# Kernel optimization log

Measured on AMD Instinct MI355X. Metric: run time of the kernel, lower is better.

## Reference

```python
import jax, jax.numpy as jnp
import numpy as np


def setup_inputs() -> dict:
    key = jax.random.key(0)
    k1, k2, k3, k4, k5 = jax.random.split(key, 5)
    B, S, H, NL = 256, 128, 768, 2
    return {
        "t_logits": jax.random.normal(k1, (B, NL), dtype=jnp.float32),
        "s_logits": jax.random.normal(k2, (B, NL), dtype=jnp.float32),
        "t_features": jax.random.normal(k3, (B, S, H), dtype=jnp.float32),
        "s_features": jax.random.normal(k4, (B, S, H), dtype=jnp.float32),
        "labels": jax.random.randint(k5, (B,), 0, NL, dtype=jnp.int64),
        "k": 5,
        "temperature": 4,
    }


def reference(t_logits, s_logits, t_features, s_features, labels, k, temperature):
    B = s_features.shape[0]
    D = s_features.shape[1] * s_features.shape[2]  # flattened feature dim S*H
    T = jnp.asarray(temperature, dtype=s_logits.dtype)

    # train_loss: standard cross-entropy computed inside the student model
    logp = jax.nn.log_softmax(s_logits, axis=-1)
    train_loss = -jnp.mean(jnp.take_along_axis(logp, labels[:, None].astype(jnp.int32), axis=1))

    # soft_loss: KL(batchmean) between temperature-softened teacher/student
    soft_targets = jax.nn.softmax(t_logits / T, axis=-1)
    log_probs = jax.nn.log_softmax(s_logits / T, axis=-1)
    soft_loss = jnp.sum(soft_targets * (jnp.log(soft_targets) - log_probs)) / B * T * T

    # distill_loss: per-sample squared distances to label-matched teacher
    # features, take k nearest (self included, dist 0), sum of per-neighbor
    # MSE = sqdist / D.
    tf = t_features.reshape(B, -1)
    sf = s_features.reshape(B, -1)
    # ||s_i - t_j||^2 via GEMM: [B, B]
    sq = (jnp.sum(sf * sf, axis=1)[:, None]
          + jnp.sum(tf * tf, axis=1)[None, :]
          - 2.0 * sf @ tf.T)
    sq = jnp.maximum(sq, 0.0)
    same = labels[:, None] == labels[None, :]
    masked = jnp.where(same, sq, jnp.inf)
    neg_top, _ = jax.lax.top_k(-masked, k)  # k smallest distances per row
    vals = -neg_top
    valid = jnp.isfinite(vals)  # handles groups smaller than k
    distill_loss = jnp.sum(jnp.where(valid, vals, 0.0)) / D

    return train_loss, soft_loss, distill_loss
```

## Files before the change

### kernel.cpp

```cpp
#include <hip/hip_runtime.h>
#include <math.h>


#define BMAC 256
#define BKF  32
#define LP   32
#define ST   (BMAC * LP)

typedef __attribute__((ext_vector_type(8))) short short8;
typedef __attribute__((ext_vector_type(4))) float f32x4;

__device__ inline unsigned pack_bf16(float a, float b) {
    unsigned ua = __float_as_uint(a), ub = __float_as_uint(b);
    ua = (ua + 0x7fffu + ((ua >> 16) & 1u)) >> 16;
    ub = (ub + 0x7fffu + ((ub >> 16) & 1u)) >> 16;
    return (ua & 0xffffu) | (ub << 16);
}

__global__ __launch_bounds__(1024) void gemm_dot_kernel(const float* __restrict__ S,
                                                        const float* __restrict__ T,
                                                        float* __restrict__ part,
                                                        float* __restrict__ spart,
                                                        float* __restrict__ tpart,
                                                        int* __restrict__ counter,
                                                        int B, int K, int KC) {
    extern __shared__ __align__(16) unsigned short smem[];

    const int tid  = threadIdx.x;
    const int bz   = blockIdx.x;
    const int kbeg = bz * KC;
    const int iters = KC / BKF;

    if (bz == 0 && tid == 0) *counter = 0;

    const int r = tid >> 2;
    const int g = tid & 3;
    int gi = r < B ? r : B - 1;
    const float* srcS = S + (size_t)gi * K + kbeg + g * 8;
    const float* srcT = T + (size_t)gi * K + kbeg + g * 8;
    const int woff = r * LP + ((g ^ (r & 3)) * 8);

    const int lane = tid & 63;
    const int wid  = tid >> 6;
    const int wm   = wid >> 2;
    const int wn   = wid & 3;
    const int l15  = lane & 15;
    const int quad = lane >> 4;
    const int xq   = (quad ^ (l15 & 3)) * 8;
    int aoff[4], boff[4];
    #pragma unroll
    for (int t = 0; t < 4; ++t) {
        aoff[t] = (wm * 64 + t * 16 + l15) * LP + xq;
        boff[t] = (wn * 64 + t * 16 + l15) * LP + xq;
    }

    f32x4 acc[4][4] = {};
    float pns = 0.f, pnt = 0.f;

    f32x4 s0 = *(const f32x4*)srcS;
    f32x4 s1 = *(const f32x4*)(srcS + 4);
    f32x4 t0 = *(const f32x4*)srcT;
    f32x4 t1 = *(const f32x4*)(srcT + 4);

    for (int it = 0; it < iters; ++it) {
        unsigned short* As = smem + (it & 1) * 2 * ST;
        unsigned short* Bs = As + ST;

        pns += s0.x*s0.x + s0.y*s0.y + s0.z*s0.z + s0.w*s0.w
             + s1.x*s1.x + s1.y*s1.y + s1.z*s1.z + s1.w*s1.w;
        pnt += t0.x*t0.x + t0.y*t0.y + t0.z*t0.z + t0.w*t0.w
             + t1.x*t1.x + t1.y*t1.y + t1.z*t1.z + t1.w*t1.w;
        uint4 pa = make_uint4(pack_bf16(s0.x, s0.y), pack_bf16(s0.z, s0.w),
                              pack_bf16(s1.x, s1.y), pack_bf16(s1.z, s1.w));
        uint4 pb = make_uint4(pack_bf16(t0.x, t0.y), pack_bf16(t0.z, t0.w),
                              pack_bf16(t1.x, t1.y), pack_bf16(t1.z, t1.w));
        *(uint4*)&As[woff] = pa;
        *(uint4*)&Bs[woff] = pb;

        if (it + 1 < iters) {
            const float* nS = srcS + (it + 1) * BKF;
            const float* nT = srcT + (it + 1) * BKF;
            s0 = *(const f32x4*)nS;
            s1 = *(const f32x4*)(nS + 4);
            t0 = *(const f32x4*)nT;
            t1 = *(const f32x4*)(nT + 4);
        }

        __syncthreads();

        short8 bfr[4];
        #pragma unroll
        for (int ni = 0; ni < 4; ++ni)
            bfr[ni] = *(const short8*)&Bs[boff[ni]];
        #pragma unroll
        for (int mi = 0; mi < 4; ++mi) {
            short8 afr = *(const short8*)&As[aoff[mi]];
            #pragma unroll
            for (int ni = 0; ni < 4; ++ni)
                acc[mi][ni] = __builtin_amdgcn_mfma_f32_16x16x32_bf16(
                    afr, bfr[ni], acc[mi][ni], 0, 0, 0);
        }
    }

    float* outp = part + (size_t)bz * B * B;
    #pragma unroll
    for (int mi = 0; mi < 4; ++mi) {
        #pragma unroll
        for (int ni = 0; ni < 4; ++ni) {
            #pragma unroll
            for (int rr = 0; rr < 4; ++rr) {
                const int ig = wm * 64 + mi * 16 + quad * 4 + rr;
                const int jg = wn * 64 + ni * 16 + l15;
                if (ig < B && jg < B)
                    outp[(size_t)ig * B + jg] = acc[mi][ni][rr];
            }
        }
    }

    {
        float v = pns;
        v += __shfl_xor(v, 1, 64);
        v += __shfl_xor(v, 2, 64);
        if ((tid & 3) == 0 && r < B) spart[(size_t)bz * B + r] = v;
        float w = pnt;
        w += __shfl_xor(w, 1, 64);
        w += __shfl_xor(w, 2, 64);
        if ((tid & 3) == 0 && r < B) tpart[(size_t)bz * B + r] = w;
    }
}

__global__ __launch_bounds__(256) void tail_kernel(const float* __restrict__ part,
                                                   const float* __restrict__ spart,
                                                   const float* __restrict__ tpart,
                                                   const float* __restrict__ t_logits,
                                                   const float* __restrict__ s_logits,
                                                   const int* __restrict__ labels,
                                                   const int* __restrict__ kp,
                                                   const int* __restrict__ tp,
                                                   float* __restrict__ rowsum,
                                                   int* __restrict__ counter,
                                                   float* __restrict__ out,
                                                   int B, int K, int NL, int gz) {
    const int i   = blockIdx.x;
    const int tid = threadIdx.x;
    const size_t BB = (size_t)B * B;

    __shared__ float svals[256];
    __shared__ float rv[256];
    __shared__ int   ri[256];
    __shared__ float red[4];
    __shared__ float snv;
    __shared__ int   lastf;

    float sp = 0.f;
    for (int z = tid; z < gz; z += 256) sp += spart[(size_t)z * B + i];
    #pragma unroll
    for (int off = 32; off > 0; off >>= 1) sp += __shfl_down(sp, off, 64);
    if ((tid & 63) == 0) red[tid >> 6] = sp;
    __syncthreads();
    if (tid == 0) snv = red[0] + red[1] + red[2] + red[3];
    __syncthreads();
    const float sn = snv;

    float v = INFINITY;
    if (tid < B) {
        const float* pp = part + (size_t)i * B + tid;
        const float* tq = tpart + tid;
        float d0=0.f,d1=0.f,d2=0.f,d3=0.f,d4=0.f,d5=0.f,d6=0.f,d7=0.f;
        float tn = 0.f;
        int z = 0;
        for (; z + 8 <= gz; z += 8) {
            d0 += pp[(size_t)(z+0) * BB];
            d1 += pp[(size_t)(z+1) * BB];
            d2 += pp[(size_t)(z+2) * BB];
            d3 += pp[(size_t)(z+3) * BB];
            d4 += pp[(size_t)(z+4) * BB];
            d5 += pp[(size_t)(z+5) * BB];
            d6 += pp[(size_t)(z+6) * BB];
            d7 += pp[(size_t)(z+7) * BB];
            tn += tq[(size_t)(z+0) * B] + tq[(size_t)(z+1) * B]
                + tq[(size_t)(z+2) * B] + tq[(size_t)(z+3) * B]
                + tq[(size_t)(z+4) * B] + tq[(size_t)(z+5) * B]
                + tq[(size_t)(z+6) * B] + tq[(size_t)(z+7) * B];
        }
        float dt = ((d0+d1)+(d2+d3)) + ((d4+d5)+(d6+d7));
        for (; z < gz; ++z) {
            dt += pp[(size_t)z * BB];
            tn += tq[(size_t)z * B];
        }
        if (labels[i] == labels[tid])
            v = fmaxf(sn + tn - 2.0f * dt, 0.0f);
    }
    svals[tid] = v;
    __syncthreads();

    const int k = kp[0];
    float sum = 0.0f;
    for (int it = 0; it < k; ++it) {
        rv[tid] = svals[tid];
        ri[tid] = tid;
        __syncthreads();
        #pragma unroll
        for (int s = 128; s > 0; s >>= 1) {
            if (tid < s) {
                if (rv[tid + s] < rv[tid]) { rv[tid] = rv[tid + s]; ri[tid] = ri[tid + s]; }
            }
            __syncthreads();
        }
        if (tid == 0) {
            if (rv[0] < 3.0e38f) sum += rv[0];
            svals[ri[0]] = INFINITY;
        }
        __syncthreads();
    }

    if (tid == 0) {
        rowsum[i] = sum;
        __threadfence();
        lastf = (atomicAdd(counter, 1) == B - 1) ? 1 : 0;
    }
    __syncthreads();
    if (!lastf) return;

    __threadfence();
    const float Tv = (float)tp[0];
    float rs = (tid < B) ? rowsum[tid] : 0.f;
    float ce = 0.0f, kl = 0.0f;
    for (int s = tid; s < B; s += 256) {
        const float* sl = s_logits + (size_t)s * NL;
        const float* tl = t_logits + (size_t)s * NL;
        float mx = -INFINITY;
        for (int c = 0; c < NL; ++c) mx = fmaxf(mx, sl[c]);
        float se = 0.0f;
        for (int c = 0; c < NL; ++c) se += expf(sl[c] - mx);
        ce += logf(se) + mx - sl[labels[s]];

        float mxs = -INFINITY, mxt = -INFINITY;
        for (int c = 0; c < NL; ++c) {
            mxs = fmaxf(mxs, sl[c] / Tv);
            mxt = fmaxf(mxt, tl[c] / Tv);
        }
        float ses = 0.0f, set = 0.0f;
        for (int c = 0; c < NL; ++c) {
            ses += expf(sl[c] / Tv - mxs);
            set += expf(tl[c] / Tv - mxt);
        }
        float lses = logf(ses) + mxs;
        float lset = logf(set) + mxt;
        for (int c = 0; c < NL; ++c) {
            float lst = tl[c] / Tv - lset;
            float ls  = sl[c] / Tv - lses;
            kl += expf(lst) * (lst - ls);
        }
    }
    #pragma unroll
    for (int off = 32; off > 0; off >>= 1) {
        ce += __shfl_down(ce, off, 64);
        kl += __shfl_down(kl, off, 64);
        rs += __shfl_down(rs, off, 64);
    }
    __shared__ float wce[4], wkl[4], wrs[4];
    if ((tid & 63) == 0) { wce[tid >> 6] = ce; wkl[tid >> 6] = kl; wrs[tid >> 6] = rs; }
    __syncthreads();
    if (tid == 0) {
        out[0] = (wce[0] + wce[1] + wce[2] + wce[3]) / (float)B;
        out[1] = (wkl[0] + wkl[1] + wkl[2] + wkl[3]) / (float)B * Tv * Tv;
        out[2] = (wrs[0] + wrs[1] + wrs[2] + wrs[3]) / (float)K;
    }
}

extern "C" void kernel_launch(void* const* d_in, const int* in_sizes, int n_in,
                              void* d_out, int out_size, void* d_ws, size_t ws_size,
                              hipStream_t stream) {
    const float* t_logits = (const float*)d_in[0];
    const float* s_logits = (const float*)d_in[1];
    const float* t_feat   = (const float*)d_in[2];
    const float* s_feat   = (const float*)d_in[3];
    const int*   labels   = (const int*)d_in[4];
    const int*   kp       = (const int*)d_in[5];
    const int*   tp       = (const int*)d_in[6];
    float* out = (float*)d_out;

    const int B  = in_sizes[4];
    const int NL = in_sizes[0] / B;
    const int K  = in_sizes[2] / B;
    const size_t BB = (size_t)B * B;

    const size_t avail = ws_size / 4;
    const int cands[] = {256, 192, 128, 96, 64, 48, 32, 24, 16, 12, 8, 6, 4};
    int gz = 4;
    for (int ci = 0; ci < 13; ++ci) {
        const int g = cands[ci];
        if (K % (g * BKF) != 0) continue;
        const size_t need = (size_t)g * BB + 2 * (size_t)g * B + B + 1;
        if (need <= avail) { gz = g; break; }
    }
    const int KC = K / gz;

    float* ws      = (float*)d_ws;
    float* part    = ws;
    float* spart   = part + (size_t)gz * BB;
    float* tpart   = spart + (size_t)gz * B;
    float* rowsum  = tpart + (size_t)gz * B;
    int*   counter = (int*)(rowsum + B);

    const size_t lds_bytes = 2 * 2 * (size_t)ST * sizeof(unsigned short);
    gemm_dot_kernel<<<gz, 1024, lds_bytes, stream>>>(s_feat, t_feat, part,
                                                     spart, tpart, counter,
                                                     B, K, KC);

    tail_kernel<<<B, 256, 0, stream>>>(part, spart, tpart, t_logits, s_logits,
                                       labels, kp, tp, rowsum, counter, out,
                                       B, K, NL, gz);
}
```

Baseline: 276.1 us.

## Tile split-K GEMM into 128x128 output blocks with XCD-aware scheduling

Replaces the one-block-per-K-slice 256x256 GEMM (1024 threads) with 128x128 output tiles handled by 256-thread blocks, so the grid becomes tiles x split-K. This raises block count and occupancy (launch bounds of 3 blocks per CU), and maps K slices to XCDs so blocks sharing inputs land on the same L2. Row norms are computed only by the tiles on the first row or column. LDS now uses padded rows (stride 40) in place of the XOR swizzle. The cost is that each input row is loaded twice across tiles, and gz drops from 256 to 192.

```diff
diff --git a/kernel.cpp b/kernel.cpp
--- a/kernel.cpp
+++ b/kernel.cpp
@@ -2,10 +2,11 @@
 #include <math.h>
 
 
-#define BMAC 256
-#define BKF  32
-#define LP   32
-#define ST   (BMAC * LP)
+#define TM 128
+#define TN 128
+#define BK 32
+#define LP 40
+#define STH (TM * LP)
 
 typedef __attribute__((ext_vector_type(8))) short short8;
 typedef __attribute__((ext_vector_type(4))) float f32x4;
@@ -17,73 +18,113 @@
     return (ua & 0xffffu) | (ub << 16);
 }
 
-__global__ __launch_bounds__(1024) void gemm_dot_kernel(const float* __restrict__ S,
-                                                        const float* __restrict__ T,
-                                                        float* __restrict__ part,
-                                                        float* __restrict__ spart,
-                                                        float* __restrict__ tpart,
-                                                        int* __restrict__ counter,
-                                                        int B, int K, int KC) {
+__global__ __launch_bounds__(256, 3) void gemm_dot_kernel(const float* __restrict__ S,
+                                                          const float* __restrict__ T,
+                                                          float* __restrict__ part,
+                                                          float* __restrict__ spart,
+                                                          float* __restrict__ tpart,
+                                                          int* __restrict__ counter,
+                                                          int B, int K, int KC,
+                                                          int mt, int nt, int gz) {
     extern __shared__ __align__(16) unsigned short smem[];
 
-    const int tid  = threadIdx.x;
-    const int bz   = blockIdx.x;
-    const int kbeg = bz * KC;
-    const int iters = KC / BKF;
-
-    if (bz == 0 && tid == 0) *counter = 0;
-
-    const int r = tid >> 2;
-    const int g = tid & 3;
-    int gi = r < B ? r : B - 1;
-    const float* srcS = S + (size_t)gi * K + kbeg + g * 8;
-    const float* srcT = T + (size_t)gi * K + kbeg + g * 8;
-    const int woff = r * LP + ((g ^ (r & 3)) * 8);
+    const int tid   = threadIdx.x;
+    const int blk   = blockIdx.x;
+    const int tiles = mt * nt;
+
+    if (blk == 0 && tid == 0) *counter = 0;
+
+    int z, mn;
+    if ((gz & 7) == 0) {
+        const int xcd  = blk & 7;
+        const int slot = blk >> 3;
+        const int zpx  = gz >> 3;
+        mn = slot % tiles;
+        z  = xcd * zpx + slot / tiles;
+    } else {
+        z  = blk / tiles;
+        mn = blk % tiles;
+    }
+    const int i0 = (mn / nt) * TM;
+    const int j0 = (mn % nt) * TN;
+    const int kbeg  = z * KC;
+    const int iters = KC / BK;
 
     const int lane = tid & 63;
     const int wid  = tid >> 6;
-    const int wm   = wid >> 2;
-    const int wn   = wid & 3;
+    const int wm   = wid >> 1;
+    const int wn   = wid & 1;
     const int l15  = lane & 15;
     const int quad = lane >> 4;
-    const int xq   = (quad ^ (l15 & 3)) * 8;
+
+    const int r = tid >> 1;
+    const int h = tid & 1;
+    int gi = i0 + r; if (gi >= B) gi = B - 1;
+    int gj = j0 + r; if (gj >= B) gj = B - 1;
+    const float* srcS = S + (size_t)gi * K + kbeg + h * 16;
+    const float* srcT = T + (size_t)gj * K + kbeg + h * 16;
+    const int woff = r * LP + h * 16;
+
     int aoff[4], boff[4];
     #pragma unroll
     for (int t = 0; t < 4; ++t) {
-        aoff[t] = (wm * 64 + t * 16 + l15) * LP + xq;
-        boff[t] = (wn * 64 + t * 16 + l15) * LP + xq;
-    }
+        aoff[t] = (wm * 64 + t * 16 + l15) * LP + quad * 8;
+        boff[t] = (wn * 64 + t * 16 + l15) * LP + quad * 8;
+    }
+
+    const bool doS = ((mn % nt) == 0);
+    const bool doT = ((mn / nt) == 0);
 
     f32x4 acc[4][4] = {};
     float pns = 0.f, pnt = 0.f;
 
-    f32x4 s0 = *(const f32x4*)srcS;
+    f32x4 s0 = *(const f32x4*)(srcS + 0);
     f32x4 s1 = *(const f32x4*)(srcS + 4);
-    f32x4 t0 = *(const f32x4*)srcT;
+    f32x4 s2 = *(const f32x4*)(srcS + 8);
+    f32x4 s3 = *(const f32x4*)(srcS + 12);
+    f32x4 t0 = *(const f32x4*)(srcT + 0);
     f32x4 t1 = *(const f32x4*)(srcT + 4);
+    f32x4 t2 = *(const f32x4*)(srcT + 8);
+    f32x4 t3 = *(const f32x4*)(srcT + 12);
 
     for (int it = 0; it < iters; ++it) {
-        unsigned short* As = smem + (it & 1) * 2 * ST;
-        unsigned short* Bs = As + ST;
-
-        pns += s0.x*s0.x + s0.y*s0.y + s0.z*s0.z + s0.w*s0.w
-             + s1.x*s1.x + s1.y*s1.y + s1.z*s1.z + s1.w*s1.w;
-        pnt += t0.x*t0.x + t0.y*t0.y + t0.z*t0.z + t0.w*t0.w
-             + t1.x*t1.x + t1.y*t1.y + t1.z*t1.z + t1.w*t1.w;
-        uint4 pa = make_uint4(pack_bf16(s0.x, s0.y), pack_bf16(s0.z, s0.w),
-                              pack_bf16(s1.x, s1.y), pack_bf16(s1.z, s1.w));
-        uint4 pb = make_uint4(pack_bf16(t0.x, t0.y), pack_bf16(t0.z, t0.w),
-                              pack_bf16(t1.x, t1.y), pack_bf16(t1.z, t1.w));
-        *(uint4*)&As[woff] = pa;
-        *(uint4*)&Bs[woff] = pb;
+        unsigned short* As = smem + (it & 1) * 2 * STH;
+        unsigned short* Bs = As + STH;
+
+        if (doS)
+            pns += s0.x*s0.x + s0.y*s0.y + s0.z*s0.z + s0.w*s0.w
+                 + s1.x*s1.x + s1.y*s1.y + s1.z*s1.z + s1.w*s1.w
+                 + s2.x*s2.x + s2.y*s2.y + s2.z*s2.z + s2.w*s2.w
+                 + s3.x*s3.x + s3.y*s3.y + s3.z*s3.z + s3.w*s3.w;
+        if (doT)
+            pnt += t0.x*t0.x + t0.y*t0.y + t0.z*t0.z + t0.w*t0.w
+                 + t1.x*t1.x + t1.y*t1.y + t1.z*t1.z + t1.w*t1.w
+                 + t2.x*t2.x + t2.y*t2.y + t2.z*t2.z + t2.w*t2.w
+                 + t3.x*t3.x + t3.y*t3.y + t3.z*t3.z + t3.w*t3.w;
+        uint4 pa0 = make_uint4(pack_bf16(s0.x, s0.y), pack_bf16(s0.z, s0.w),
+                               pack_bf16(s1.x, s1.y), pack_bf16(s1.z, s1.w));
+        uint4 pa1 = make_uint4(pack_bf16(s2.x, s2.y), pack_bf16(s2.z, s2.w),
+                               pack_bf16(s3.x, s3.y), pack_bf16(s3.z, s3.w));
+        uint4 pb0 = make_uint4(pack_bf16(t0.x, t0.y), pack_bf16(t0.z, t0.w),
+                               pack_bf16(t1.x, t1.y), pack_bf16(t1.z, t1.w));
+        uint4 pb1 = make_uint4(pack_bf16(t2.x, t2.y), pack_bf16(t2.z, t2.w),
+                               pack_bf16(t3.x, t3.y), pack_bf16(t3.z, t3.w));
+        *(uint4*)&As[woff]     = pa0;
+        *(uint4*)&As[woff + 8] = pa1;
+        *(uint4*)&Bs[woff]     = pb0;
+        *(uint4*)&Bs[woff + 8] = pb1;
 
         if (it + 1 < iters) {
-            const float* nS = srcS + (it + 1) * BKF;
-            const float* nT = srcT + (it + 1) * BKF;
-            s0 = *(const f32x4*)nS;
+            const float* nS = srcS + (it + 1) * BK;
+            const float* nT = srcT + (it + 1) * BK;
+            s0 = *(const f32x4*)(nS + 0);
             s1 = *(const f32x4*)(nS + 4);
-            t0 = *(const f32x4*)nT;
+            s2 = *(const f32x4*)(nS + 8);
+            s3 = *(const f32x4*)(nS + 12);
+            t0 = *(const f32x4*)(nT + 0);
             t1 = *(const f32x4*)(nT + 4);
+            t2 = *(const f32x4*)(nT + 8);
+            t3 = *(const f32x4*)(nT + 12);
         }
 
         __syncthreads();
@@ -102,30 +143,28 @@
         }
     }
 
-    float* outp = part + (size_t)bz * B * B;
+    float* outp = part + (size_t)z * B * B;
     #pragma unroll
     for (int mi = 0; mi < 4; ++mi) {
         #pragma unroll
         for (int ni = 0; ni < 4; ++ni) {
             #pragma unroll
             for (int rr = 0; rr < 4; ++rr) {
-                const int ig = wm * 64 + mi * 16 + quad * 4 + rr;
-                const int jg = wn * 64 + ni * 16 + l15;
+                const int ig = i0 + wm * 64 + mi * 16 + quad * 4 + rr;
+                const int jg = j0 + wn * 64 + ni * 16 + l15;
                 if (ig < B && jg < B)
                     outp[(size_t)ig * B + jg] = acc[mi][ni][rr];
             }
         }
     }
 
-    {
-        float v = pns;
-        v += __shfl_xor(v, 1, 64);
-        v += __shfl_xor(v, 2, 64);
-        if ((tid & 3) == 0 && r < B) spart[(size_t)bz * B + r] = v;
-        float w = pnt;
-        w += __shfl_xor(w, 1, 64);
-        w += __shfl_xor(w, 2, 64);
-        if ((tid & 3) == 0 && r < B) tpart[(size_t)bz * B + r] = w;
+    if (doS) {
+        float v = pns + __shfl_xor(pns, 1, 64);
+        if (h == 0 && i0 + r < B) spart[(size_t)z * B + i0 + r] = v;
+    }
+    if (doT) {
+        float v = pnt + __shfl_xor(pnt, 1, 64);
+        if (h == 0 && j0 + r < B) tpart[(size_t)z * B + j0 + r] = v;
     }
 }
 
@@ -286,12 +325,15 @@
     const int K  = in_sizes[2] / B;
     const size_t BB = (size_t)B * B;
 
+    const int mt = (B + TM - 1) / TM;
+    const int nt = (B + TN - 1) / TN;
+
     const size_t avail = ws_size / 4;
-    const int cands[] = {256, 192, 128, 96, 64, 48, 32, 24, 16, 12, 8, 6, 4};
-    int gz = 4;
-    for (int ci = 0; ci < 13; ++ci) {
+    const int cands[] = {192, 128, 96, 64, 48, 32, 24, 16, 12, 8, 6, 4, 2, 1};
+    int gz = 1;
+    for (int ci = 0; ci < 14; ++ci) {
         const int g = cands[ci];
-        if (K % (g * BKF) != 0) continue;
+        if (K % (g * BK) != 0) continue;
         const size_t need = (size_t)g * BB + 2 * (size_t)g * B + B + 1;
         if (need <= avail) { gz = g; break; }
     }
@@ -304,10 +346,11 @@
     float* rowsum  = tpart + (size_t)gz * B;
     int*   counter = (int*)(rowsum + B);
 
-    const size_t lds_bytes = 2 * 2 * (size_t)ST * sizeof(unsigned short);
-    gemm_dot_kernel<<<gz, 1024, lds_bytes, stream>>>(s_feat, t_feat, part,
-                                                     spart, tpart, counter,
-                                                     B, K, KC);
+    const int grid = mt * nt * gz;
+    const size_t lds_bytes = 2 * 2 * (size_t)STH * sizeof(unsigned short);
+    gemm_dot_kernel<<<grid, 256, lds_bytes, stream>>>(s_feat, t_feat, part,
+                                                      spart, tpart, counter,
+                                                      B, K, KC, mt, nt, gz);
 
     tail_kernel<<<B, 256, 0, stream>>>(part, spart, tpart, t_logits, s_logits,
                                        labels, kp, tp, rowsum, counter, out,
```

New measurement: 268.6 us. -2.7%, faster.
